# Optimization experiments

Measured on AMD Instinct MI355X. Metric: run time of the kernel, lower is better.

The kernel has to match this reference:

```python
import jax, jax.numpy as jnp
import numpy as np

B, C, Cs, CI, H, W = 4, 256, 256, 128, 64, 64

def setup_inputs() -> dict:
    key = jax.random.key(0)
    ks = jax.random.split(key, 9)
    sq = 1.0 / np.sqrt(C)
    ss = 1.0 / np.sqrt(Cs)
    return {
        "x_main": jax.random.normal(ks[0], (B, C, H, W), jnp.float32),
        "z_p": jax.random.normal(ks[1], (B, Cs, H, W), jnp.float32),
        "Wq": jax.random.normal(ks[2], (CI, C), jnp.float32) * sq,
        "bq": jax.random.normal(ks[3], (CI,), jnp.float32) * 0.01,
        "Wk": jax.random.normal(ks[4], (CI, Cs), jnp.float32) * ss,
        "bk": jax.random.normal(ks[5], (CI,), jnp.float32) * 0.01,
        "Wv": jax.random.normal(ks[6], (C, Cs), jnp.float32) * ss,
        "bv": jax.random.normal(ks[7], (C,), jnp.float32) * 0.01,
        "gamma": jax.random.normal(ks[8], (1,), jnp.float32) * 0.1,
    }

def reference(x_main, z_p, Wq, bq, Wk, bk, Wv, bv, gamma):
    b, c, h, w = x_main.shape
    n = h * w
    xm = x_main.reshape(b, c, n)          # [B, C, N]
    zf = z_p.reshape(b, z_p.shape[1], n)  # [B, Cs, M] (M == N here)
    # 1x1 convs == per-pixel channel projections
    q = jnp.einsum('oc,bcn->bon', Wq, xm) + bq[None, :, None]  # [B, CI, N]
    k = jnp.einsum('oc,bcm->bom', Wk, zf) + bk[None, :, None]  # [B, CI, M]
    v = jnp.einsum('oc,bcm->bom', Wv, zf) + bv[None, :, None]  # [B, C, M]
    # energy[b, n, m] = q_n . k_m  (no scaling, as in the original)
    energy = jnp.einsum('bcn,bcm->bnm', q, k)
    attention = jax.nn.softmax(energy, axis=-1)
    out = jnp.einsum('bom,bnm->bon', v, attention)  # [B, C, N]
    out = out.reshape(b, c, h, w)
    return gamma * out + x_main
```

## Files before the change

### kernel.cpp

```cpp
#include <hip/hip_runtime.h>
#include <hip/hip_bf16.h>


typedef __bf16  bf16x8  __attribute__((ext_vector_type(8)));
typedef float   f32x16  __attribute__((ext_vector_type(16)));

#define LOG2E 1.4426950408889634f

union BF8 { __hip_bfloat162 h[4]; bf16x8 v; };
union U4  { unsigned u[4]; bf16x8 v; };

__device__ inline bf16x8 pack8(const float f[8]) {
  BF8 u;
#pragma unroll
  for (int i = 0; i < 4; i++)
    u.h[i] = __float22bfloat162_rn(float2{f[2 * i], f[2 * i + 1]});
  return u.v;
}

__device__ inline void dma16(const void* g, void* l) {
  __builtin_amdgcn_global_load_lds(
      (const __attribute__((address_space(1))) unsigned int*)g,
      (__attribute__((address_space(3))) unsigned int*)l, 16, 0, 0);
}

__global__ __launch_bounds__(256) void prep_kernel(
    const float* __restrict__ x, const float* __restrict__ z,
    const float* __restrict__ Wq, const float* __restrict__ Wk,
    const float* __restrict__ Wv,
    __hip_bfloat16* __restrict__ xf, __hip_bfloat16* __restrict__ zf,
    __hip_bfloat16* __restrict__ wfr)
{
  __shared__ float lds[256 * 68];
  const int bi = blockIdx.x;
  const int tid = threadIdx.x;
  if (bi < 512) {
    const int sel = bi >> 8;
    const int b   = (bi >> 6) & 3;
    const int pc  = bi & 63;
    const float* in = sel ? z : x;
    __hip_bfloat16* outp = sel ? zf : xf;
    const size_t ib = (size_t)b * 256 * 4096 + pc * 64;
    const int pix4 = (tid & 15) * 4;
#pragma unroll
    for (int it = 0; it < 16; it++) {
      int ch = it * 16 + (tid >> 4);
      float4 v4 = *(const float4*)&in[ib + (size_t)ch * 4096 + pix4];
      *(float4*)&lds[ch * 68 + pix4] = v4;
    }
    __syncthreads();
    const size_t ob = ((size_t)(b * 128 + pc * 2)) * 8192;
#pragma unroll
    for (int i = 0; i < 8; i++) {
      int c = i * 256 + tid;
      int grp = c >> 10, cs = (c >> 6) & 15, rem = c & 63;
      int hf = rem >> 5, l32 = rem & 31;
      float f[8];
      int chb = cs * 16 + hf * 8;
#pragma unroll
      for (int j = 0; j < 8; j++)
        f[j] = lds[(chb + j) * 68 + grp * 32 + l32];
      *(bf16x8*)(outp + ob + grp * 8192 + cs * 512 + hf * 256 + l32 * 8) =
          pack8(f);
    }
  } else {
    const int base = (bi - 512) * 4096;
#pragma unroll
    for (int i = 0; i < 16; i++) {
      int c = base + i * 256 + tid;
      const float* Ws; __hip_bfloat16* dst; int rc;
      if (c < 4096)      { Ws = Wq; dst = wfr;          rc = c; }
      else if (c < 8192) { Ws = Wk; dst = wfr + 32768;  rc = c - 4096; }
      else               { Ws = Wv; dst = wfr + 65536;  rc = c - 8192; }
      int ot = rc >> 10, cs = (rc >> 6) & 15, rem = rc & 63;
      int hf = rem >> 5, l32 = rem & 31;
      const float* src = Ws + (ot * 32 + l32) * 256 + cs * 16 + hf * 8;
      float f[8];
#pragma unroll
      for (int j = 0; j < 8; j++) f[j] = src[j];
      *(bf16x8*)(dst + ot * 8192 + cs * 512 + hf * 256 + l32 * 8) = pack8(f);
    }
  }
}

__global__ __launch_bounds__(256, 2) void proj_mfma(
    const __hip_bfloat16* __restrict__ xf, const __hip_bfloat16* __restrict__ zf,
    const __hip_bfloat16* __restrict__ wfr,
    const float* __restrict__ bq, const float* __restrict__ bk,
    const float* __restrict__ bv,
    __hip_bfloat16* __restrict__ qp, __hip_bfloat16* __restrict__ kp,
    __hip_bfloat16* __restrict__ vp)
{
  const int bi = blockIdx.x;
  int mode, b, pc, h = 0;
  if (bi < 256) { mode = bi >> 7; b = (bi >> 5) & 3; pc = bi & 31; }
  else { int j = bi - 256; mode = 2; b = j >> 6; pc = (j >> 1) & 31; h = j & 1; }
  const int tid = threadIdx.x, w = tid >> 6, lane = tid & 63,
            l32 = lane & 31, half = lane >> 5;

  const __hip_bfloat16* X = (mode == 0) ? xf : zf;
  const int wtile = (mode == 2 ? h * 4 : 0) + w;
  const int wbase = (mode == 0) ? 0 : (mode == 1) ? 32768 : 65536;
  const __hip_bfloat16* wp = wfr + wbase + wtile * 8192 + lane * 8;
  bf16x8 wfg[16];
#pragma unroll
  for (int cs = 0; cs < 16; cs++) wfg[cs] = *(const bf16x8*)(wp + cs * 512);

  const float* bias = (mode == 0) ? bq : (mode == 1) ? bk : bv;
  const int ochb = (mode == 2 ? h * 128 : 0) + w * 32;
  float bb[16];
#pragma unroll
  for (int r = 0; r < 16; r++)
    bb[r] = bias[ochb + (r & 3) + 8 * (r >> 2) + 4 * half];

  const int t4 = (l32 >> 2) & 3;
  const int kperm = (t4 == 1 || t4 == 2) ? (l32 ^ 12) : l32;

#pragma unroll 1
  for (int itp = 0; itp < 2; itp++) {
    const int pg0 = pc * 4 + itp * 2;
    const __hip_bfloat16* xb0 = X + ((size_t)(b * 128 + pg0)) * 8192 + lane * 8;
    const __hip_bfloat16* xb1 = xb0 + 8192;
    f32x16 O0 = {}, O1 = {};
#pragma unroll
    for (int cs = 0; cs < 16; cs++) {
      bf16x8 xr0 = *(const bf16x8*)(xb0 + cs * 512);
      bf16x8 xr1 = *(const bf16x8*)(xb1 + cs * 512);
      O0 = __builtin_amdgcn_mfma_f32_32x32x16_bf16(wfg[cs], xr0, O0, 0, 0, 0);
      O1 = __builtin_amdgcn_mfma_f32_32x32x16_bf16(wfg[cs], xr1, O1, 0, 0, 0);
    }
#pragma unroll
    for (int p = 0; p < 2; p++) {
      const f32x16& O = p ? O1 : O0;
      const int pg = pg0 + p;
      if (mode == 0) {
        __hip_bfloat16* qb = qp + ((size_t)(b * 128 + pg)) * 4096;
#pragma unroll
        for (int r = 0; r < 16; r++) {
          int oc = ochb + (r & 3) + 8 * (r >> 2) + 4 * half;
          qb[(oc >> 4) * 512 + ((oc >> 3) & 1) * 256 + l32 * 8 + (oc & 7)] =
              __float2bfloat16((O[r] + bb[r]) * LOG2E);
        }
      } else if (mode == 1) {
        __hip_bfloat16* kb = kp + ((size_t)(b * 128 + pg)) * 4096;
#pragma unroll
        for (int r = 0; r < 16; r++) {
          int oc = ochb + (r & 3) + 8 * (r >> 2) + 4 * half;
          kb[(oc >> 4) * 512 + ((oc >> 3) & 1) * 256 + kperm * 8 + (oc & 7)] =
              __float2bfloat16(O[r] + bb[r]);
        }
      } else {
        __hip_bfloat16* vb = vp + ((size_t)(b * 128 + pg)) * 8192
            + (h * 4 + w) * 1024 + (l32 >> 4) * 512 + ((l32 >> 3) & 1) * 256
            + (l32 & 7);
#pragma unroll
        for (int r = 0; r < 16; r++) {
          int rr = (r & 3) + 8 * (r >> 2) + 4 * half;
          vb[rr * 8] = __float2bfloat16(O[r] + bb[r]);
        }
      }
    }
  }
}

struct AttnSmem {
  union {
    __hip_bfloat16 kbuf[2][8192];
    float ostage[256][33];
  } u;
  float redu[4][32];
  float rinv[32];
};

__global__ __launch_bounds__(256, 3) void attn_kernel(
    const __hip_bfloat16* __restrict__ qv, const __hip_bfloat16* __restrict__ kv,
    const __hip_bfloat16* __restrict__ vv,
    const float* __restrict__ x_main, const float* __restrict__ gammap,
    float* __restrict__ out)
{
  __shared__ AttnSmem sm;
  const int i  = blockIdx.x;
  const int b  = (i & 7) >> 1;
  const int qt = ((i >> 3) << 1) | (i & 1);
  const int n0 = qt * 32;
  const int tid  = threadIdx.x;
  const int w    = tid >> 6, lane = tid & 63, l32 = lane & 31;
  const int kh   = w >> 1, chh = w & 1;
  const int t0   = qt & 63;

  bf16x8 qf[8];
  {
    const __hip_bfloat16* qb = qv + ((size_t)(b * 128 + qt)) * 4096 + lane * 8;
#pragma unroll
    for (int cs = 0; cs < 8; cs++) qf[cs] = *(const bf16x8*)(qb + cs * 512);
  }

  const __hip_bfloat16* kg = kv + (size_t)(b * 128) * 4096;
  const __hip_bfloat16* vg = vv + (size_t)(b * 128) * 8192;

  auto stage = [&](int ta, int par) {
    __hip_bfloat16* kd = sm.u.kbuf[par];
    const __hip_bfloat16* ksrc = kg + (size_t)ta * 8192 + lane * 8;
#pragma unroll
    for (int c = 0; c < 4; c++) {
      int ck = w * 4 + c;
      dma16(ksrc + ck * 512, kd + ck * 512 + lane * 8);
    }
  };

  f32x16 Oacc[4];
#pragma unroll
  for (int c = 0; c < 4; c++)
#pragma unroll
    for (int r = 0; r < 16; r++) Oacc[c][r] = 0.f;

  float l_lane = 0.f;

  auto body = [&](int par, int ta) {
    const __hip_bfloat16* vb = vg + (size_t)(ta * 2 + kh) * 8192
                             + chh * 4096 + lane * 8;
    bf16x8 Vc[8];
#pragma unroll
    for (int c = 0; c < 4; c++) {
      Vc[2 * c]     = *(const bf16x8*)(vb + c * 1024);
      Vc[2 * c + 1] = *(const bf16x8*)(vb + c * 1024 + 512);
    }
    const __hip_bfloat16* kbase = sm.u.kbuf[par] + kh * 4096 + lane * 8;
    f32x16 S = {};
#pragma unroll
    for (int cs = 0; cs < 8; cs++) {
      bf16x8 kf = *(const bf16x8*)(kbase + cs * 512);
      S = __builtin_amdgcn_mfma_f32_32x32x16_bf16(kf, qf[cs], S, 0, 0, 0);
    }
    unsigned p2[8];
    float lsub = 0.f;
#pragma unroll
    for (int i2 = 0; i2 < 8; i2++) {
      float a = exp2f(S[2 * i2]     - 64.0f);
      float c = exp2f(S[2 * i2 + 1] - 64.0f);
      lsub += a + c;
      union { __hip_bfloat162 h; unsigned u; } cv;
      cv.h = __float22bfloat162_rn(float2{a, c});
      p2[i2] = cv.u;
    }
    l_lane += lsub;
    U4 f0, f1;
    f0.u[0] = p2[0]; f0.u[1] = p2[1]; f0.u[2] = p2[2]; f0.u[3] = p2[3];
    f1.u[0] = p2[4]; f1.u[1] = p2[5]; f1.u[2] = p2[6]; f1.u[3] = p2[7];
    const bf16x8 pf0 = f0.v, pf1 = f1.v;
#pragma unroll
    for (int c = 0; c < 4; c++) {
      Oacc[c] = __builtin_amdgcn_mfma_f32_32x32x16_bf16(Vc[2 * c],     pf0, Oacc[c], 0, 0, 0);
      Oacc[c] = __builtin_amdgcn_mfma_f32_32x32x16_bf16(Vc[2 * c + 1], pf1, Oacc[c], 0, 0, 0);
    }
  };

  stage(t0, 0);
  __syncthreads();
  stage((t0 + 1) & 63, 1);
  body(0, t0);
#pragma unroll 1
  for (int lt = 1; lt < 64; ++lt) {
    __syncthreads();
    if (lt < 63) stage((lt + 1 + t0) & 63, (lt + 1) & 1);
    body(lt & 1, (lt + t0) & 63);
  }

  float lfull = l_lane + __shfl_xor(l_lane, 32);
  if (lane < 32) sm.redu[w][l32] = lfull;
  __syncthreads();
  const int hb = lane >> 5;
  if (kh == 0) {
#pragma unroll
    for (int c = 0; c < 4; c++) {
#pragma unroll
      for (int r = 0; r < 16; r++) {
        int ch = (chh * 4 + c) * 32 + (r & 3) + 8 * (r >> 2) + 4 * hb;
        sm.u.ostage[ch][l32] = Oacc[c][r];
      }
    }
  }
  if (tid < 32) sm.rinv[tid] = 1.0f / (sm.redu[0][tid] + sm.redu[2][tid]);
  __syncthreads();
  if (kh == 1) {
#pragma unroll
    for (int c = 0; c < 4; c++) {
#pragma unroll
      for (int r = 0; r < 16; r++) {
        int ch = (chh * 4 + c) * 32 + (r & 3) + 8 * (r >> 2) + 4 * hb;
        sm.u.ostage[ch][l32] += Oacc[c][r];
      }
    }
  }
  __syncthreads();

  const float gmm = gammap[0];
  const int pix = tid & 31;
  const float ri = sm.rinv[pix];
#pragma unroll
  for (int j = 0; j < 32; ++j) {
    int ch = (tid >> 5) * 32 + j;
    size_t g = ((size_t)(b * 256 + ch)) * 4096 + n0 + pix;
    out[g] = gmm * sm.u.ostage[ch][pix] * ri + x_main[g];
  }
}

extern "C" void kernel_launch(void* const* d_in, const int* in_sizes, int n_in,
                              void* d_out, int out_size, void* d_ws, size_t ws_size,
                              hipStream_t stream) {
  (void)in_sizes; (void)n_in; (void)out_size; (void)ws_size;
  const float* x  = (const float*)d_in[0];
  const float* z  = (const float*)d_in[1];
  const float* Wq = (const float*)d_in[2];
  const float* bq = (const float*)d_in[3];
  const float* Wk = (const float*)d_in[4];
  const float* bk = (const float*)d_in[5];
  const float* Wv = (const float*)d_in[6];
  const float* bv = (const float*)d_in[7];
  const float* gm = (const float*)d_in[8];
  float* out = (float*)d_out;

  char* ws = (char*)d_ws;
  const size_t MB = 1024 * 1024;
  __hip_bfloat16* qp  = (__hip_bfloat16*)(ws);
  __hip_bfloat16* kp  = (__hip_bfloat16*)(ws + 4 * MB);
  __hip_bfloat16* vp  = (__hip_bfloat16*)(ws + 8 * MB);
  __hip_bfloat16* xfp = (__hip_bfloat16*)(ws + 16 * MB);
  __hip_bfloat16* zfp = (__hip_bfloat16*)(ws + 24 * MB);
  __hip_bfloat16* wfp = (__hip_bfloat16*)(ws + 32 * MB);

  prep_kernel<<<516, 256, 0, stream>>>(x, z, Wq, Wk, Wv, xfp, zfp, wfp);
  proj_mfma  <<<512, 256, 0, stream>>>(xfp, zfp, wfp, bq, bk, bv, qp, kp, vp);
  attn_kernel<<<512, 256, 0, stream>>>(qp, kp, vp, x, gm, out);
}
```

Baseline: 211.9 us.

## Split attention key range across six wave-pairs and read K directly from global

The attention kernel grows from 256 to 768 threads. Six wave-pairs each own a strided subset of the 128 key tiles, where before two halves walked the whole range together under block-wide syncs with double-buffered K staged into LDS by DMA. Q now lives in LDS and K is read straight from global memory, so the main loop has no barriers, and the PV MFMAs run under raised wave priority. The partial outputs are merged through LDS atomics and the softmax denominators are summed across all six groups. This trades more parallel work per block and the removal of the per-iteration syncs for extra global or L2 traffic on K, higher register pressure at 768 threads, and atomic contention in the reduction.

```diff
diff --git a/kernel.cpp b/kernel.cpp
--- a/kernel.cpp
+++ b/kernel.cpp
@@ -16,12 +16,6 @@
   for (int i = 0; i < 4; i++)
     u.h[i] = __float22bfloat162_rn(float2{f[2 * i], f[2 * i + 1]});
   return u.v;
-}
-
-__device__ inline void dma16(const void* g, void* l) {
-  __builtin_amdgcn_global_load_lds(
-      (const __attribute__((address_space(1))) unsigned int*)g,
-      (__attribute__((address_space(3))) unsigned int*)l, 16, 0, 0);
 }
 
 __global__ __launch_bounds__(256) void prep_kernel(
@@ -164,15 +158,13 @@
 }
 
 struct AttnSmem {
-  union {
-    __hip_bfloat16 kbuf[2][8192];
-    float ostage[256][33];
-  } u;
-  float redu[4][32];
+  __hip_bfloat16 qlds[4096];
+  float ost[256][33];
+  float redu[12][32];
   float rinv[32];
 };
 
-__global__ __launch_bounds__(256, 3) void attn_kernel(
+__global__ __launch_bounds__(768, 3) void attn_kernel(
     const __hip_bfloat16* __restrict__ qv, const __hip_bfloat16* __restrict__ kv,
     const __hip_bfloat16* __restrict__ vv,
     const float* __restrict__ x_main, const float* __restrict__ gammap,
@@ -184,29 +176,17 @@
   const int qt = ((i >> 3) << 1) | (i & 1);
   const int n0 = qt * 32;
   const int tid  = threadIdx.x;
-  const int w    = tid >> 6, lane = tid & 63, l32 = lane & 31;
-  const int kh   = w >> 1, chh = w & 1;
-  const int t0   = qt & 63;
-
-  bf16x8 qf[8];
-  {
-    const __hip_bfloat16* qb = qv + ((size_t)(b * 128 + qt)) * 4096 + lane * 8;
-#pragma unroll
-    for (int cs = 0; cs < 8; cs++) qf[cs] = *(const bf16x8*)(qb + cs * 512);
-  }
+  const int w    = tid >> 6, lane = tid & 63, l32 = lane & 31, hb = lane >> 5;
+  const int kl   = w >> 1, chh = w & 1;
+
+  if (tid < 512)
+    *(bf16x8*)(sm.qlds + tid * 8) =
+        *(const bf16x8*)(qv + ((size_t)(b * 128 + qt)) * 4096 + tid * 8);
+  __syncthreads();
 
   const __hip_bfloat16* kg = kv + (size_t)(b * 128) * 4096;
   const __hip_bfloat16* vg = vv + (size_t)(b * 128) * 8192;
-
-  auto stage = [&](int ta, int par) {
-    __hip_bfloat16* kd = sm.u.kbuf[par];
-    const __hip_bfloat16* ksrc = kg + (size_t)ta * 8192 + lane * 8;
-#pragma unroll
-    for (int c = 0; c < 4; c++) {
-      int ck = w * 4 + c;
-      dma16(ksrc + ck * 512, kd + ck * 512 + lane * 8);
-    }
-  };
+  const __hip_bfloat16* qb = sm.qlds + lane * 8;
 
   f32x16 Oacc[4];
 #pragma unroll
@@ -216,22 +196,32 @@
 
   float l_lane = 0.f;
 
-  auto body = [&](int par, int ta) {
-    const __hip_bfloat16* vb = vg + (size_t)(ta * 2 + kh) * 8192
-                             + chh * 4096 + lane * 8;
+  const int L = (kl < 2) ? 22 : 21;
+  int kj = (qt * 3 + kl) % L;
+
+#pragma unroll 1
+  for (int j = 0; j < L; ++j) {
+    const int s = kl + 6 * kj;
+    ++kj; if (kj == L) kj = 0;
+
+    const __hip_bfloat16* kb = kg + (size_t)s * 4096 + lane * 8;
+    const __hip_bfloat16* vb = vg + (size_t)s * 8192 + chh * 4096 + lane * 8;
+
     bf16x8 Vc[8];
 #pragma unroll
     for (int c = 0; c < 4; c++) {
       Vc[2 * c]     = *(const bf16x8*)(vb + c * 1024);
       Vc[2 * c + 1] = *(const bf16x8*)(vb + c * 1024 + 512);
     }
-    const __hip_bfloat16* kbase = sm.u.kbuf[par] + kh * 4096 + lane * 8;
+
     f32x16 S = {};
 #pragma unroll
     for (int cs = 0; cs < 8; cs++) {
-      bf16x8 kf = *(const bf16x8*)(kbase + cs * 512);
-      S = __builtin_amdgcn_mfma_f32_32x32x16_bf16(kf, qf[cs], S, 0, 0, 0);
-    }
+      bf16x8 kf = *(const bf16x8*)(kb + cs * 512);
+      bf16x8 qf = *(const bf16x8*)(qb + cs * 512);
+      S = __builtin_amdgcn_mfma_f32_32x32x16_bf16(kf, qf, S, 0, 0, 0);
+    }
+
     unsigned p2[8];
     float lsub = 0.f;
 #pragma unroll
@@ -248,60 +238,52 @@
     f0.u[0] = p2[0]; f0.u[1] = p2[1]; f0.u[2] = p2[2]; f0.u[3] = p2[3];
     f1.u[0] = p2[4]; f1.u[1] = p2[5]; f1.u[2] = p2[6]; f1.u[3] = p2[7];
     const bf16x8 pf0 = f0.v, pf1 = f1.v;
+
+    __builtin_amdgcn_s_setprio(1);
 #pragma unroll
     for (int c = 0; c < 4; c++) {
       Oacc[c] = __builtin_amdgcn_mfma_f32_32x32x16_bf16(Vc[2 * c],     pf0, Oacc[c], 0, 0, 0);
       Oacc[c] = __builtin_amdgcn_mfma_f32_32x32x16_bf16(Vc[2 * c + 1], pf1, Oacc[c], 0, 0, 0);
     }
-  };
-
-  stage(t0, 0);
-  __syncthreads();
-  stage((t0 + 1) & 63, 1);
-  body(0, t0);
-#pragma unroll 1
-  for (int lt = 1; lt < 64; ++lt) {
-    __syncthreads();
-    if (lt < 63) stage((lt + 1 + t0) & 63, (lt + 1) & 1);
-    body(lt & 1, (lt + t0) & 63);
+    __builtin_amdgcn_s_setprio(0);
   }
 
   float lfull = l_lane + __shfl_xor(l_lane, 32);
   if (lane < 32) sm.redu[w][l32] = lfull;
   __syncthreads();
-  const int hb = lane >> 5;
-  if (kh == 0) {
-#pragma unroll
-    for (int c = 0; c < 4; c++) {
+
+  if (kl == 0) {
+#pragma unroll
+    for (int c = 0; c < 4; c++)
 #pragma unroll
       for (int r = 0; r < 16; r++) {
         int ch = (chh * 4 + c) * 32 + (r & 3) + 8 * (r >> 2) + 4 * hb;
-        sm.u.ostage[ch][l32] = Oacc[c][r];
+        sm.ost[ch][l32] = Oacc[c][r];
       }
-    }
-  }
-  if (tid < 32) sm.rinv[tid] = 1.0f / (sm.redu[0][tid] + sm.redu[2][tid]);
+  }
+  if (tid < 32) {
+    float t = sm.redu[0][tid] + sm.redu[2][tid] + sm.redu[4][tid]
+            + sm.redu[6][tid] + sm.redu[8][tid] + sm.redu[10][tid];
+    sm.rinv[tid] = 1.0f / t;
+  }
   __syncthreads();
-  if (kh == 1) {
-#pragma unroll
-    for (int c = 0; c < 4; c++) {
+  if (kl != 0) {
+#pragma unroll
+    for (int c = 0; c < 4; c++)
 #pragma unroll
       for (int r = 0; r < 16; r++) {
         int ch = (chh * 4 + c) * 32 + (r & 3) + 8 * (r >> 2) + 4 * hb;
-        sm.u.ostage[ch][l32] += Oacc[c][r];
+        atomicAdd(&sm.ost[ch][l32], Oacc[c][r]);
       }
-    }
   }
   __syncthreads();
 
   const float gmm = gammap[0];
-  const int pix = tid & 31;
-  const float ri = sm.rinv[pix];
-#pragma unroll
-  for (int j = 0; j < 32; ++j) {
-    int ch = (tid >> 5) * 32 + j;
+#pragma unroll 1
+  for (int idx = tid; idx < 8192; idx += 768) {
+    int ch = idx >> 5, pix = idx & 31;
     size_t g = ((size_t)(b * 256 + ch)) * 4096 + n0 + pix;
-    out[g] = gmm * sm.u.ostage[ch][pix] * ri + x_main[g];
+    out[g] = gmm * sm.ost[ch][pix] * sm.rinv[pix] + x_main[g];
   }
 }
 
@@ -331,5 +313,5 @@
 
   prep_kernel<<<516, 256, 0, stream>>>(x, z, Wq, Wk, Wv, xfp, zfp, wfp);
   proj_mfma  <<<512, 256, 0, stream>>>(xfp, zfp, wfp, bq, bk, bv, qp, kp, vp);
-  attn_kernel<<<512, 256, 0, stream>>>(qp, kp, vp, x, gm, out);
-}
+  attn_kernel<<<512, 768, 0, stream>>>(qp, kp, vp, x, gm, out);
+}
```

Result: slower. 321.9 us (+51.9%).

## Split attention over key range with merge kernel; double projection grid

Applied to the files above, without the earlier changes.

Splits the attention key loop into two halves processed by separate blocks (1024 blocks instead of 512), writing unnormalized partial outputs and row sums to workspace, then a merge kernel combines them, normalizes, scales by gamma and adds the residual. The projection kernel also drops its two-iteration loop so it launches twice as many blocks, with a higher occupancy hint. The aim is better CU occupancy and load balance on a large-CU GPU, at the cost of an extra kernel launch and about 32 MB of fp32 partial traffic. Because softmax here uses no running max, the two halves can be summed directly. The split path runs only if the workspace holds at least 66 MB.

```diff
diff --git a/kernel.cpp b/kernel.cpp
--- a/kernel.cpp
+++ b/kernel.cpp
@@ -83,7 +83,7 @@
   }
 }
 
-__global__ __launch_bounds__(256, 2) void proj_mfma(
+__global__ __launch_bounds__(256, 3) void proj_mfma(
     const __hip_bfloat16* __restrict__ xf, const __hip_bfloat16* __restrict__ zf,
     const __hip_bfloat16* __restrict__ wfr,
     const float* __restrict__ bq, const float* __restrict__ bk,
@@ -92,9 +92,9 @@
     __hip_bfloat16* __restrict__ vp)
 {
   const int bi = blockIdx.x;
-  int mode, b, pc, h = 0;
-  if (bi < 256) { mode = bi >> 7; b = (bi >> 5) & 3; pc = bi & 31; }
-  else { int j = bi - 256; mode = 2; b = j >> 6; pc = (j >> 1) & 31; h = j & 1; }
+  int mode, b, pg0, h = 0;
+  if (bi < 512) { mode = bi >> 8; b = (bi >> 6) & 3; pg0 = (bi & 63) * 2; }
+  else { int j = bi - 512; mode = 2; b = j >> 7; pg0 = ((j >> 1) & 63) * 2; h = j & 1; }
   const int tid = threadIdx.x, w = tid >> 6, lane = tid & 63,
             l32 = lane & 31, half = lane >> 5;
 
@@ -116,48 +116,44 @@
   const int t4 = (l32 >> 2) & 3;
   const int kperm = (t4 == 1 || t4 == 2) ? (l32 ^ 12) : l32;
 
-#pragma unroll 1
-  for (int itp = 0; itp < 2; itp++) {
-    const int pg0 = pc * 4 + itp * 2;
-    const __hip_bfloat16* xb0 = X + ((size_t)(b * 128 + pg0)) * 8192 + lane * 8;
-    const __hip_bfloat16* xb1 = xb0 + 8192;
-    f32x16 O0 = {}, O1 = {};
-#pragma unroll
-    for (int cs = 0; cs < 16; cs++) {
-      bf16x8 xr0 = *(const bf16x8*)(xb0 + cs * 512);
-      bf16x8 xr1 = *(const bf16x8*)(xb1 + cs * 512);
-      O0 = __builtin_amdgcn_mfma_f32_32x32x16_bf16(wfg[cs], xr0, O0, 0, 0, 0);
-      O1 = __builtin_amdgcn_mfma_f32_32x32x16_bf16(wfg[cs], xr1, O1, 0, 0, 0);
-    }
-#pragma unroll
-    for (int p = 0; p < 2; p++) {
-      const f32x16& O = p ? O1 : O0;
-      const int pg = pg0 + p;
-      if (mode == 0) {
-        __hip_bfloat16* qb = qp + ((size_t)(b * 128 + pg)) * 4096;
-#pragma unroll
-        for (int r = 0; r < 16; r++) {
-          int oc = ochb + (r & 3) + 8 * (r >> 2) + 4 * half;
-          qb[(oc >> 4) * 512 + ((oc >> 3) & 1) * 256 + l32 * 8 + (oc & 7)] =
-              __float2bfloat16((O[r] + bb[r]) * LOG2E);
-        }
-      } else if (mode == 1) {
-        __hip_bfloat16* kb = kp + ((size_t)(b * 128 + pg)) * 4096;
-#pragma unroll
-        for (int r = 0; r < 16; r++) {
-          int oc = ochb + (r & 3) + 8 * (r >> 2) + 4 * half;
-          kb[(oc >> 4) * 512 + ((oc >> 3) & 1) * 256 + kperm * 8 + (oc & 7)] =
-              __float2bfloat16(O[r] + bb[r]);
-        }
-      } else {
-        __hip_bfloat16* vb = vp + ((size_t)(b * 128 + pg)) * 8192
-            + (h * 4 + w) * 1024 + (l32 >> 4) * 512 + ((l32 >> 3) & 1) * 256
-            + (l32 & 7);
-#pragma unroll
-        for (int r = 0; r < 16; r++) {
-          int rr = (r & 3) + 8 * (r >> 2) + 4 * half;
-          vb[rr * 8] = __float2bfloat16(O[r] + bb[r]);
-        }
+  const __hip_bfloat16* xb0 = X + ((size_t)(b * 128 + pg0)) * 8192 + lane * 8;
+  const __hip_bfloat16* xb1 = xb0 + 8192;
+  f32x16 O0 = {}, O1 = {};
+#pragma unroll
+  for (int cs = 0; cs < 16; cs++) {
+    bf16x8 xr0 = *(const bf16x8*)(xb0 + cs * 512);
+    bf16x8 xr1 = *(const bf16x8*)(xb1 + cs * 512);
+    O0 = __builtin_amdgcn_mfma_f32_32x32x16_bf16(wfg[cs], xr0, O0, 0, 0, 0);
+    O1 = __builtin_amdgcn_mfma_f32_32x32x16_bf16(wfg[cs], xr1, O1, 0, 0, 0);
+  }
+#pragma unroll
+  for (int p = 0; p < 2; p++) {
+    const f32x16& O = p ? O1 : O0;
+    const int pg = pg0 + p;
+    if (mode == 0) {
+      __hip_bfloat16* qb = qp + ((size_t)(b * 128 + pg)) * 4096;
+#pragma unroll
+      for (int r = 0; r < 16; r++) {
+        int oc = ochb + (r & 3) + 8 * (r >> 2) + 4 * half;
+        qb[(oc >> 4) * 512 + ((oc >> 3) & 1) * 256 + l32 * 8 + (oc & 7)] =
+            __float2bfloat16((O[r] + bb[r]) * LOG2E);
+      }
+    } else if (mode == 1) {
+      __hip_bfloat16* kb = kp + ((size_t)(b * 128 + pg)) * 4096;
+#pragma unroll
+      for (int r = 0; r < 16; r++) {
+        int oc = ochb + (r & 3) + 8 * (r >> 2) + 4 * half;
+        kb[(oc >> 4) * 512 + ((oc >> 3) & 1) * 256 + kperm * 8 + (oc & 7)] =
+            __float2bfloat16(O[r] + bb[r]);
+      }
+    } else {
+      __hip_bfloat16* vb = vp + ((size_t)(b * 128 + pg)) * 8192
+          + (h * 4 + w) * 1024 + (l32 >> 4) * 512 + ((l32 >> 3) & 1) * 256
+          + (l32 & 7);
+#pragma unroll
+      for (int r = 0; r < 16; r++) {
+        int rr = (r & 3) + 8 * (r >> 2) + 4 * half;
+        vb[rr * 8] = __float2bfloat16(O[r] + bb[r]);
       }
     }
   }
@@ -172,21 +168,27 @@
   float rinv[32];
 };
 
+template <int SPLIT>
 __global__ __launch_bounds__(256, 3) void attn_kernel(
     const __hip_bfloat16* __restrict__ qv, const __hip_bfloat16* __restrict__ kv,
     const __hip_bfloat16* __restrict__ vv,
     const float* __restrict__ x_main, const float* __restrict__ gammap,
-    float* __restrict__ out)
+    float* __restrict__ out,
+    float* __restrict__ part, float* __restrict__ lpart)
 {
   __shared__ AttnSmem sm;
   const int i  = blockIdx.x;
   const int b  = (i & 7) >> 1;
-  const int qt = ((i >> 3) << 1) | (i & 1);
+  int qt, kt2;
+  if (SPLIT) { int j = i >> 3; kt2 = j >> 6; qt = ((j & 63) << 1) | (i & 1); }
+  else       { kt2 = 0;        qt = ((i >> 3) << 1) | (i & 1); }
+  const int NT = SPLIT ? 32 : 64;
+  const int sbase = kt2 * 32;
   const int n0 = qt * 32;
   const int tid  = threadIdx.x;
   const int w    = tid >> 6, lane = tid & 63, l32 = lane & 31;
   const int kh   = w >> 1, chh = w & 1;
-  const int t0   = qt & 63;
+  const int t0   = qt & (NT - 1);
 
   bf16x8 qf[8];
   {
@@ -200,7 +202,7 @@
 
   auto stage = [&](int ta, int par) {
     __hip_bfloat16* kd = sm.u.kbuf[par];
-    const __hip_bfloat16* ksrc = kg + (size_t)ta * 8192 + lane * 8;
+    const __hip_bfloat16* ksrc = kg + (size_t)(sbase + ta) * 8192 + lane * 8;
 #pragma unroll
     for (int c = 0; c < 4; c++) {
       int ck = w * 4 + c;
@@ -217,7 +219,7 @@
   float l_lane = 0.f;
 
   auto body = [&](int par, int ta) {
-    const __hip_bfloat16* vb = vg + (size_t)(ta * 2 + kh) * 8192
+    const __hip_bfloat16* vb = vg + (size_t)((sbase + ta) * 2 + kh) * 8192
                              + chh * 4096 + lane * 8;
     bf16x8 Vc[8];
 #pragma unroll
@@ -257,19 +259,20 @@
 
   stage(t0, 0);
   __syncthreads();
-  stage((t0 + 1) & 63, 1);
+  stage((t0 + 1) & (NT - 1), 1);
   body(0, t0);
 #pragma unroll 1
-  for (int lt = 1; lt < 64; ++lt) {
+  for (int lt = 1; lt < NT; ++lt) {
     __syncthreads();
-    if (lt < 63) stage((lt + 1 + t0) & 63, (lt + 1) & 1);
-    body(lt & 1, (lt + t0) & 63);
+    if (lt < NT - 1) stage((lt + 1 + t0) & (NT - 1), (lt + 1) & 1);
+    body(lt & 1, (lt + t0) & (NT - 1));
   }
 
   float lfull = l_lane + __shfl_xor(l_lane, 32);
   if (lane < 32) sm.redu[w][l32] = lfull;
   __syncthreads();
   const int hb = lane >> 5;
+  const int pblk = SPLIT ? ((b * 128 + qt) * 2 + kt2) : 0;
   if (kh == 0) {
 #pragma unroll
     for (int c = 0; c < 4; c++) {
@@ -280,7 +283,12 @@
       }
     }
   }
-  if (tid < 32) sm.rinv[tid] = 1.0f / (sm.redu[0][tid] + sm.redu[2][tid]);
+  if (SPLIT) {
+    if (tid < 32)
+      lpart[(size_t)pblk * 32 + tid] = sm.redu[0][tid] + sm.redu[2][tid];
+  } else {
+    if (tid < 32) sm.rinv[tid] = 1.0f / (sm.redu[0][tid] + sm.redu[2][tid]);
+  }
   __syncthreads();
   if (kh == 1) {
 #pragma unroll
@@ -294,21 +302,50 @@
   }
   __syncthreads();
 
-  const float gmm = gammap[0];
   const int pix = tid & 31;
-  const float ri = sm.rinv[pix];
+  if (SPLIT) {
+    float* pb = part + (size_t)pblk * 8192;
+#pragma unroll
+    for (int j = 0; j < 32; ++j) {
+      int ch = (tid >> 5) * 32 + j;
+      pb[ch * 32 + pix] = sm.u.ostage[ch][pix];
+    }
+  } else {
+    const float gmm = gammap[0];
+    const float ri = sm.rinv[pix];
+#pragma unroll
+    for (int j = 0; j < 32; ++j) {
+      int ch = (tid >> 5) * 32 + j;
+      size_t g = ((size_t)(b * 256 + ch)) * 4096 + n0 + pix;
+      out[g] = gmm * sm.u.ostage[ch][pix] * ri + x_main[g];
+    }
+  }
+}
+
+__global__ __launch_bounds__(256) void merge_kernel(
+    const float* __restrict__ part, const float* __restrict__ lpart,
+    const float* __restrict__ x_main, const float* __restrict__ gammap,
+    float* __restrict__ out)
+{
+  const int i = blockIdx.x;
+  const int b = i >> 7, qt = i & 127, n0 = qt * 32;
+  const int tid = threadIdx.x, pix = tid & 31;
+  const size_t pb = (size_t)((b * 128 + qt) * 2) * 8192;
+  const float* lp = lpart + (size_t)((b * 128 + qt) * 2) * 32;
+  const float rv = gammap[0] / (lp[pix] + lp[32 + pix]);
 #pragma unroll
   for (int j = 0; j < 32; ++j) {
     int ch = (tid >> 5) * 32 + j;
     size_t g = ((size_t)(b * 256 + ch)) * 4096 + n0 + pix;
-    out[g] = gmm * sm.u.ostage[ch][pix] * ri + x_main[g];
+    float o = (part[pb + ch * 32 + pix] + part[pb + 8192 + ch * 32 + pix]) * rv;
+    out[g] = o + x_main[g];
   }
 }
 
 extern "C" void kernel_launch(void* const* d_in, const int* in_sizes, int n_in,
                               void* d_out, int out_size, void* d_ws, size_t ws_size,
                               hipStream_t stream) {
-  (void)in_sizes; (void)n_in; (void)out_size; (void)ws_size;
+  (void)in_sizes; (void)n_in; (void)out_size;
   const float* x  = (const float*)d_in[0];
   const float* z  = (const float*)d_in[1];
   const float* Wq = (const float*)d_in[2];
@@ -328,8 +365,17 @@
   __hip_bfloat16* xfp = (__hip_bfloat16*)(ws + 16 * MB);
   __hip_bfloat16* zfp = (__hip_bfloat16*)(ws + 24 * MB);
   __hip_bfloat16* wfp = (__hip_bfloat16*)(ws + 32 * MB);
+  float* part  = (float*)(ws + 33 * MB);
+  float* lpart = (float*)(ws + 65 * MB);
+
+  const bool split = ws_size >= 66 * MB;
 
   prep_kernel<<<516, 256, 0, stream>>>(x, z, Wq, Wk, Wv, xfp, zfp, wfp);
-  proj_mfma  <<<512, 256, 0, stream>>>(xfp, zfp, wfp, bq, bk, bv, qp, kp, vp);
-  attn_kernel<<<512, 256, 0, stream>>>(qp, kp, vp, x, gm, out);
-}
+  proj_mfma  <<<1024, 256, 0, stream>>>(xfp, zfp, wfp, bq, bk, bv, qp, kp, vp);
+  if (split) {
+    attn_kernel<1><<<1024, 256, 0, stream>>>(qp, kp, vp, x, gm, out, part, lpart);
+    merge_kernel<<<512, 256, 0, stream>>>(part, lpart, x, gm, out);
+  } else {
+    attn_kernel<0><<<512, 256, 0, stream>>>(qp, kp, vp, x, gm, out, part, lpart);
+  }
+}
```

New measurement: 219.7 us. 3.7% more time.

## Software-pipeline attention loop across tiles and double projection grid size

Applied to the files above, without the earlier changes.

The attention main loop is split into load-V, QK, softmax and PV stages and software-pipelined, so the PV MFMAs of the previous tile overlap the QK and exp work of the current one, with V loads double-buffered in registers. The goal is to hide MFMA and exp latency within a wave. Holding more live registers, attention launch bounds drop from 3 to 2 blocks per CU, trading occupancy for instruction-level overlap. Separately, the projection kernel runs 1024 blocks with one pixel-pair per block instead of two iterations, and its occupancy hint is raised to 3.

```diff
diff --git a/kernel.cpp b/kernel.cpp
--- a/kernel.cpp
+++ b/kernel.cpp
@@ -83,7 +83,7 @@
   }
 }
 
-__global__ __launch_bounds__(256, 2) void proj_mfma(
+__global__ __launch_bounds__(256, 3) void proj_mfma(
     const __hip_bfloat16* __restrict__ xf, const __hip_bfloat16* __restrict__ zf,
     const __hip_bfloat16* __restrict__ wfr,
     const float* __restrict__ bq, const float* __restrict__ bk,
@@ -92,9 +92,9 @@
     __hip_bfloat16* __restrict__ vp)
 {
   const int bi = blockIdx.x;
-  int mode, b, pc, h = 0;
-  if (bi < 256) { mode = bi >> 7; b = (bi >> 5) & 3; pc = bi & 31; }
-  else { int j = bi - 256; mode = 2; b = j >> 6; pc = (j >> 1) & 31; h = j & 1; }
+  int mode, b, pg0, h = 0;
+  if (bi < 512) { mode = bi >> 8; b = (bi >> 6) & 3; pg0 = (bi & 63) * 2; }
+  else { int j = bi - 512; mode = 2; b = j >> 7; pg0 = ((j >> 1) & 63) * 2; h = j & 1; }
   const int tid = threadIdx.x, w = tid >> 6, lane = tid & 63,
             l32 = lane & 31, half = lane >> 5;
 
@@ -116,48 +116,44 @@
   const int t4 = (l32 >> 2) & 3;
   const int kperm = (t4 == 1 || t4 == 2) ? (l32 ^ 12) : l32;
 
-#pragma unroll 1
-  for (int itp = 0; itp < 2; itp++) {
-    const int pg0 = pc * 4 + itp * 2;
-    const __hip_bfloat16* xb0 = X + ((size_t)(b * 128 + pg0)) * 8192 + lane * 8;
-    const __hip_bfloat16* xb1 = xb0 + 8192;
-    f32x16 O0 = {}, O1 = {};
-#pragma unroll
-    for (int cs = 0; cs < 16; cs++) {
-      bf16x8 xr0 = *(const bf16x8*)(xb0 + cs * 512);
-      bf16x8 xr1 = *(const bf16x8*)(xb1 + cs * 512);
-      O0 = __builtin_amdgcn_mfma_f32_32x32x16_bf16(wfg[cs], xr0, O0, 0, 0, 0);
-      O1 = __builtin_amdgcn_mfma_f32_32x32x16_bf16(wfg[cs], xr1, O1, 0, 0, 0);
-    }
-#pragma unroll
-    for (int p = 0; p < 2; p++) {
-      const f32x16& O = p ? O1 : O0;
-      const int pg = pg0 + p;
-      if (mode == 0) {
-        __hip_bfloat16* qb = qp + ((size_t)(b * 128 + pg)) * 4096;
-#pragma unroll
-        for (int r = 0; r < 16; r++) {
-          int oc = ochb + (r & 3) + 8 * (r >> 2) + 4 * half;
-          qb[(oc >> 4) * 512 + ((oc >> 3) & 1) * 256 + l32 * 8 + (oc & 7)] =
-              __float2bfloat16((O[r] + bb[r]) * LOG2E);
-        }
-      } else if (mode == 1) {
-        __hip_bfloat16* kb = kp + ((size_t)(b * 128 + pg)) * 4096;
-#pragma unroll
-        for (int r = 0; r < 16; r++) {
-          int oc = ochb + (r & 3) + 8 * (r >> 2) + 4 * half;
-          kb[(oc >> 4) * 512 + ((oc >> 3) & 1) * 256 + kperm * 8 + (oc & 7)] =
-              __float2bfloat16(O[r] + bb[r]);
-        }
-      } else {
-        __hip_bfloat16* vb = vp + ((size_t)(b * 128 + pg)) * 8192
-            + (h * 4 + w) * 1024 + (l32 >> 4) * 512 + ((l32 >> 3) & 1) * 256
-            + (l32 & 7);
-#pragma unroll
-        for (int r = 0; r < 16; r++) {
-          int rr = (r & 3) + 8 * (r >> 2) + 4 * half;
-          vb[rr * 8] = __float2bfloat16(O[r] + bb[r]);
-        }
+  const __hip_bfloat16* xb0 = X + ((size_t)(b * 128 + pg0)) * 8192 + lane * 8;
+  const __hip_bfloat16* xb1 = xb0 + 8192;
+  f32x16 O0 = {}, O1 = {};
+#pragma unroll
+  for (int cs = 0; cs < 16; cs++) {
+    bf16x8 xr0 = *(const bf16x8*)(xb0 + cs * 512);
+    bf16x8 xr1 = *(const bf16x8*)(xb1 + cs * 512);
+    O0 = __builtin_amdgcn_mfma_f32_32x32x16_bf16(wfg[cs], xr0, O0, 0, 0, 0);
+    O1 = __builtin_amdgcn_mfma_f32_32x32x16_bf16(wfg[cs], xr1, O1, 0, 0, 0);
+  }
+#pragma unroll
+  for (int p = 0; p < 2; p++) {
+    const f32x16& O = p ? O1 : O0;
+    const int pg = pg0 + p;
+    if (mode == 0) {
+      __hip_bfloat16* qb = qp + ((size_t)(b * 128 + pg)) * 4096;
+#pragma unroll
+      for (int r = 0; r < 16; r++) {
+        int oc = ochb + (r & 3) + 8 * (r >> 2) + 4 * half;
+        qb[(oc >> 4) * 512 + ((oc >> 3) & 1) * 256 + l32 * 8 + (oc & 7)] =
+            __float2bfloat16((O[r] + bb[r]) * LOG2E);
+      }
+    } else if (mode == 1) {
+      __hip_bfloat16* kb = kp + ((size_t)(b * 128 + pg)) * 4096;
+#pragma unroll
+      for (int r = 0; r < 16; r++) {
+        int oc = ochb + (r & 3) + 8 * (r >> 2) + 4 * half;
+        kb[(oc >> 4) * 512 + ((oc >> 3) & 1) * 256 + kperm * 8 + (oc & 7)] =
+            __float2bfloat16(O[r] + bb[r]);
+      }
+    } else {
+      __hip_bfloat16* vb = vp + ((size_t)(b * 128 + pg)) * 8192
+          + (h * 4 + w) * 1024 + (l32 >> 4) * 512 + ((l32 >> 3) & 1) * 256
+          + (l32 & 7);
+#pragma unroll
+      for (int r = 0; r < 16; r++) {
+        int rr = (r & 3) + 8 * (r >> 2) + 4 * half;
+        vb[rr * 8] = __float2bfloat16(O[r] + bb[r]);
       }
     }
   }
@@ -172,7 +168,7 @@
   float rinv[32];
 };
 
-__global__ __launch_bounds__(256, 3) void attn_kernel(
+__global__ __launch_bounds__(256, 2) void attn_kernel(
     const __hip_bfloat16* __restrict__ qv, const __hip_bfloat16* __restrict__ kv,
     const __hip_bfloat16* __restrict__ vv,
     const float* __restrict__ x_main, const float* __restrict__ gammap,
@@ -216,15 +212,17 @@
 
   float l_lane = 0.f;
 
-  auto body = [&](int par, int ta) {
+  auto loadV = [&](int ta, bf16x8* Vc) {
     const __hip_bfloat16* vb = vg + (size_t)(ta * 2 + kh) * 8192
                              + chh * 4096 + lane * 8;
-    bf16x8 Vc[8];
 #pragma unroll
     for (int c = 0; c < 4; c++) {
       Vc[2 * c]     = *(const bf16x8*)(vb + c * 1024);
       Vc[2 * c + 1] = *(const bf16x8*)(vb + c * 1024 + 512);
     }
+  };
+
+  auto qk = [&](int par) -> f32x16 {
     const __hip_bfloat16* kbase = sm.u.kbuf[par] + kh * 4096 + lane * 8;
     f32x16 S = {};
 #pragma unroll
@@ -232,6 +230,10 @@
       bf16x8 kf = *(const bf16x8*)(kbase + cs * 512);
       S = __builtin_amdgcn_mfma_f32_32x32x16_bf16(kf, qf[cs], S, 0, 0, 0);
     }
+    return S;
+  };
+
+  auto softmax = [&](const f32x16& S, bf16x8& pf0, bf16x8& pf1) {
     unsigned p2[8];
     float lsub = 0.f;
 #pragma unroll
@@ -247,7 +249,10 @@
     U4 f0, f1;
     f0.u[0] = p2[0]; f0.u[1] = p2[1]; f0.u[2] = p2[2]; f0.u[3] = p2[3];
     f1.u[0] = p2[4]; f1.u[1] = p2[5]; f1.u[2] = p2[6]; f1.u[3] = p2[7];
-    const bf16x8 pf0 = f0.v, pf1 = f1.v;
+    pf0 = f0.v; pf1 = f1.v;
+  };
+
+  auto pv = [&](const bf16x8* Vc, bf16x8 pf0, bf16x8 pf1) {
 #pragma unroll
     for (int c = 0; c < 4; c++) {
       Oacc[c] = __builtin_amdgcn_mfma_f32_32x32x16_bf16(Vc[2 * c],     pf0, Oacc[c], 0, 0, 0);
@@ -255,16 +260,45 @@
     }
   };
 
+  bf16x8 VcA[8], VcB[8];
+  bf16x8 pf0, pf1;
+
   stage(t0, 0);
   __syncthreads();
   stage((t0 + 1) & 63, 1);
-  body(0, t0);
+  loadV(t0, VcA);
+  {
+    f32x16 S = qk(0);
+    softmax(S, pf0, pf1);
+  }
+
 #pragma unroll 1
-  for (int lt = 1; lt < 64; ++lt) {
+  for (int lt = 1; lt < 63; lt += 2) {
     __syncthreads();
-    if (lt < 63) stage((lt + 1 + t0) & 63, (lt + 1) & 1);
-    body(lt & 1, (lt + t0) & 63);
-  }
+    stage((lt + 1 + t0) & 63, 0);
+    loadV((lt + t0) & 63, VcB);
+    {
+      f32x16 S = qk(1);
+      pv(VcA, pf0, pf1);
+      softmax(S, pf0, pf1);
+    }
+    __syncthreads();
+    stage((lt + 2 + t0) & 63, 1);
+    loadV((lt + 1 + t0) & 63, VcA);
+    {
+      f32x16 S = qk(0);
+      pv(VcB, pf0, pf1);
+      softmax(S, pf0, pf1);
+    }
+  }
+  __syncthreads();
+  loadV((63 + t0) & 63, VcB);
+  {
+    f32x16 S = qk(1);
+    pv(VcA, pf0, pf1);
+    softmax(S, pf0, pf1);
+  }
+  pv(VcB, pf0, pf1);
 
   float lfull = l_lane + __shfl_xor(l_lane, 32);
   if (lane < 32) sm.redu[w][l32] = lfull;
@@ -330,6 +364,6 @@
   __hip_bfloat16* wfp = (__hip_bfloat16*)(ws + 32 * MB);
 
   prep_kernel<<<516, 256, 0, stream>>>(x, z, Wq, Wk, Wv, xfp, zfp, wfp);
-  proj_mfma  <<<512, 256, 0, stream>>>(xfp, zfp, wfp, bq, bk, bv, qp, kp, vp);
+  proj_mfma  <<<1024, 256, 0, stream>>>(xfp, zfp, wfp, bq, bk, bv, qp, kp, vp);
   attn_kernel<<<512, 256, 0, stream>>>(qp, kp, vp, x, gm, out);
 }
```

After: 212.6 us. About the same (+0.3%).
